# Performance work log

Measured on AMD Instinct MI355X. Metric: run time of the kernel, lower is better.

Reference implementation:

```python
import jax, jax.numpy as jnp
import numpy as np
from math import sqrt

D_MODEL = 1024
N_HEADS = 16
FFN = 4096
B, N = 2, 2048
EPS = 1e-5


def _layernorm(x, g, b):
    mu = jnp.mean(x, -1, keepdims=True)
    var = jnp.mean((x - mu) ** 2, -1, keepdims=True)
    return (x - mu) * jax.lax.rsqrt(var + EPS) * g + b


def setup_inputs() -> dict:
    key = jax.random.key(0)
    ks = jax.random.split(key, 12)
    s = 1.0 / sqrt(D_MODEL)
    sf = 1.0 / sqrt(FFN)
    inp = {
        "tgt": jax.random.normal(ks[0], (B, N, D_MODEL), jnp.float32),
        # True = masked. Causal: query i may attend to keys j <= i.
        "tgt_mask": jnp.triu(jnp.ones((N, N), jnp.bool_), k=1),
        "tgt_key_pad_mask": jnp.zeros((B, N), jnp.bool_),
        "Wq": jax.random.uniform(ks[1], (D_MODEL, D_MODEL), jnp.float32, -s, s),
        "Wk": jax.random.uniform(ks[2], (D_MODEL, D_MODEL), jnp.float32, -s, s),
        "Wv": jax.random.uniform(ks[3], (D_MODEL, D_MODEL), jnp.float32, -s, s),
        "Wo": jax.random.uniform(ks[4], (D_MODEL, D_MODEL), jnp.float32, -s, s),
        "bo": jax.random.uniform(ks[5], (D_MODEL,), jnp.float32, -s, s),
        "W1": jax.random.uniform(ks[6], (FFN, D_MODEL), jnp.float32, -s, s),
        "b1": jax.random.uniform(ks[7], (FFN,), jnp.float32, -s, s),
        "W2": jax.random.uniform(ks[8], (D_MODEL, FFN), jnp.float32, -sf, sf),
        "b2": jax.random.uniform(ks[9], (D_MODEL,), jnp.float32, -sf, sf),
        "g1": jnp.ones((D_MODEL,), jnp.float32),
        "beta1": jnp.zeros((D_MODEL,), jnp.float32),
        "g2": jnp.ones((D_MODEL,), jnp.float32),
        "beta2": jnp.zeros((D_MODEL,), jnp.float32),
    }
    return inp


def _mha(x, tgt_mask, pad_mask, Wq, Wk, Wv, Wo, bo):
    b, n, d = x.shape
    dk = d // N_HEADS
    q = (x @ Wq.T).reshape(b, n, N_HEADS, dk).transpose(0, 2, 1, 3)  # bhnd
    k = (x @ Wk.T).reshape(b, n, N_HEADS, dk).transpose(0, 2, 1, 3)
    v = (x @ Wv.T).reshape(b, n, N_HEADS, dk).transpose(0, 2, 1, 3)
    scores = jnp.einsum("bhqd,bhkd->bhqk", q, k) / sqrt(dk)
    mask = tgt_mask[None, None, :, :] | pad_mask[:, None, None, :]
    scores = jnp.where(mask, -jnp.inf, scores)
    att = jax.nn.softmax(scores, axis=-1)
    out = jnp.einsum("bhqk,bhkd->bhqd", att, v).transpose(0, 2, 1, 3).reshape(b, n, d)
    return out @ Wo.T + bo


def reference(tgt, tgt_mask, tgt_key_pad_mask, Wq, Wk, Wv, Wo, bo,
              W1, b1, W2, b2, g1, beta1, g2, beta2):
    # PostNorm logic (pre_norm=False), dropout=0 (eval)
    h = _mha(tgt, tgt_mask, tgt_key_pad_mask, Wq, Wk, Wv, Wo, bo)
    x = _layernorm(tgt + h, g1, beta1)
    m = jax.nn.gelu(x @ W1.T + b1, approximate=True) @ W2.T + b2
    return _layernorm(x + m, g2, beta2)
```

## Files before the change

kernel.cpp:

```cpp
#include <hip/hip_runtime.h>


#define DEV __device__ __forceinline__

typedef __attribute__((ext_vector_type(4)))  float f32x4;
typedef __attribute__((ext_vector_type(16))) float f32x16;
typedef __attribute__((ext_vector_type(8)))  short s16x8;

static constexpr int Bb   = 2;
static constexpr int NN   = 2048;
static constexpr int DM   = 1024;
static constexpr int HH   = 16;
static constexpr int DK   = 64;
static constexpr int FF   = 4096;
static constexpr int ROWS = Bb * NN;

#define AS1(p) ((const __attribute__((address_space(1))) void*)(p))
#define AS3(p) ((__attribute__((address_space(3))) void*)(p))

DEV unsigned short f2bf(float f) {
  unsigned u = __float_as_uint(f);
  u += 0x7fff + ((u >> 16) & 1);
  return (unsigned short)(u >> 16);
}
DEV float fexp2(float x) {
  float r;
  asm("v_exp_f32 %0, %1" : "=v"(r) : "v"(x));
  return r;
}
DEV unsigned cvtpk(float lo, float hi) {
  unsigned r;
  asm("v_cvt_pk_bf16_f32 %0, %1, %2" : "=v"(r) : "v"(lo), "v"(hi));
  return r;
}

__global__ __launch_bounds__(256) void k_cast7(
    const float* __restrict__ tgt, const float* __restrict__ Wq,
    const float* __restrict__ Wk, const float* __restrict__ Wv,
    const float* __restrict__ Wo, const float* __restrict__ W1,
    const float* __restrict__ W2,
    ushort* __restrict__ xb, ushort* __restrict__ wqb,
    ushort* __restrict__ w1b, ushort* __restrict__ w2b) {
  const int i = blockIdx.x * 256 + threadIdx.x;
  constexpr int S0 = 1048576;
  constexpr int S1 = 262144;
  const float4* src;
  ushort* dstp;
  if (i < S0)               { src = (const float4*)tgt + i;            dstp = xb  + (size_t)i * 4; }
  else if (i < S0 + S1)     { src = (const float4*)Wq + (i - S0);      dstp = wqb + (size_t)(i - S0) * 4; }
  else if (i < S0 + 2 * S1) { src = (const float4*)Wk + (i - S0 - S1); dstp = wqb + (size_t)(i - S0) * 4; }
  else if (i < S0 + 3 * S1) { src = (const float4*)Wv + (i - S0 - 2 * S1); dstp = wqb + (size_t)(i - S0) * 4; }
  else if (i < S0 + 4 * S1) { src = (const float4*)Wo + (i - S0 - 3 * S1); dstp = wqb + (size_t)(i - S0) * 4; }
  else if (i < 3 * S0)      { src = (const float4*)W1 + (i - 2 * S0);  dstp = w1b + (size_t)(i - 2 * S0) * 4; }
  else                      { src = (const float4*)W2 + (i - 3 * S0);  dstp = w2b + (size_t)(i - 3 * S0) * 4; }
  float4 v = *src;
  ushort4 o;
  o.x = f2bf(v.x); o.y = f2bf(v.y); o.z = f2bf(v.z); o.w = f2bf(v.w);
  *reinterpret_cast<ushort4*>(dstp) = o;
}

template <int EPI, int BN, bool QKV>
__global__ __launch_bounds__(256) void k_gemm(
    const ushort* __restrict__ A, const ushort* __restrict__ Bt,
    const float* __restrict__ bias, const float* __restrict__ resid,
    ushort* __restrict__ Cb, float* __restrict__ Cf,
    int K, int nbx) {
  __shared__ ushort As[2][128][32];
  __shared__ ushort Bs[2][BN][32];

  const int t = threadIdx.x;
  const int lane = t & 63, w = t >> 6;
  const int lr = lane & 15, lg = lane >> 4;
  const int lrow = lane >> 2, lc8 = (lane & 3) * 8;

  const int nwg = gridDim.x;
  const int bid = blockIdx.x;
  const int q8 = nwg >> 3, r8 = nwg & 7;
  const int xcd = bid & 7, lin = bid >> 3;
  const int wg = (xcd < r8 ? xcd * (q8 + 1) : r8 * (q8 + 1) + (xcd - r8) * q8) + lin;
  const int band = wg / (4 * nbx);
  const int inn  = wg % (4 * nbx);
  const int by = band * 4 + (inn & 3);
  const int bx = inn >> 2;

  const int bRow = by * 128;
  const int bCol = bx * BN;

  constexpr int NW = BN / 32;
  const int wRow = (w >> 1) * 64, wCol = (w & 1) * (BN / 2);

  const f32x4 zero = {0.f, 0.f, 0.f, 0.f};
  f32x4 acc[4][NW];
#pragma unroll
  for (int m = 0; m < 4; ++m)
#pragma unroll
    for (int n = 0; n < NW; ++n) acc[m][n] = zero;

  auto stage = [&](int buf, int kt) {
#pragma unroll
    for (int i = 0; i < 2; ++i) {
      int rr = w * 32 + i * 16;
      __builtin_amdgcn_global_load_lds(
          AS1(A + (size_t)(bRow + rr + lrow) * K + kt + lc8),
          AS3(&As[buf][rr][0]), 16, 0, 0);
    }
#pragma unroll
    for (int i = 0; i < BN / 64; ++i) {
      int rr = w * (BN / 4) + i * 16;
      __builtin_amdgcn_global_load_lds(
          AS1(Bt + (size_t)(bCol + rr + lrow) * K + kt + lc8),
          AS3(&Bs[buf][rr][0]), 16, 0, 0);
    }
  };

  stage(0, 0);
  const int nk = K / 32;
  for (int tt = 0; tt < nk; ++tt) {
    const int cur = tt & 1;
    __syncthreads();
    if (tt + 1 < nk) stage(cur ^ 1, (tt + 1) * 32);

    s16x8 af[4], bfr[NW];
#pragma unroll
    for (int m = 0; m < 4; ++m)
      af[m] = *reinterpret_cast<const s16x8*>(&As[cur][wRow + m * 16 + lr][lg * 8]);
#pragma unroll
    for (int n = 0; n < NW; ++n)
      bfr[n] = *reinterpret_cast<const s16x8*>(&Bs[cur][wCol + n * 16 + lr][lg * 8]);
#pragma unroll
    for (int m = 0; m < 4; ++m)
#pragma unroll
      for (int n = 0; n < NW; ++n)
        acc[m][n] = __builtin_amdgcn_mfma_f32_16x16x32_bf16(af[m], bfr[n], acc[m][n], 0, 0, 0);
  }

  ushort* CbOut = Cb;
  int colBase = bCol, Ncols = nbx * BN, third = 0;
  if (QKV) {
    third = bCol >> 10;
    CbOut = Cb + (size_t)third * ROWS * DM;
    colBase = bCol & 1023;
    Ncols = DM;
  }
#pragma unroll
  for (int m = 0; m < 4; ++m) {
    int gr = bRow + wRow + m * 16 + lg * 4;
#pragma unroll
    for (int n = 0; n < NW; ++n) {
      int gc = colBase + wCol + n * 16 + lr;
      float bv = (EPI == 1 || EPI == 2) ? bias[gc] : 0.0f;
#pragma unroll
      for (int r = 0; r < 4; ++r) {
        int nr = gr + r;
        float v = acc[m][n][r] + bv;
        if (EPI == 2) {
          size_t idx = (size_t)nr * Ncols + gc;
          Cf[idx] = v + resid[idx];
        } else if (EPI == 1) {
          size_t idx = (size_t)nr * Ncols + gc;
          float u = v + 0.044715f * v * v * v;
          float g = v / (1.0f + __expf(-1.5957691216057308f * u));
          CbOut[idx] = f2bf(g);
        } else {
          int gcs = gc;
          if (QKV && third == 1)
            gcs = (gc & ~63) | ((gc ^ ((nr & 7) << 3)) & 63);
          CbOut[(size_t)nr * Ncols + gcs] = f2bf(v);
        }
      }
    }
  }
}

__global__ __launch_bounds__(256) void k_vt(const ushort* __restrict__ V,
                                            ushort* __restrict__ vT) {
  __shared__ ushort Ls[64][72];
  const int t = threadIdx.x;
  const int n0 = blockIdx.x * 64;
  const int bh = blockIdx.y;
  const int b = bh >> 4, h = bh & 15;
  const int n = t >> 2;
#pragma unroll
  for (int half = 0; half < 2; ++half) {
    int c8 = ((t & 3) + half * 4) * 8;
    int4 v = *reinterpret_cast<const int4*>(
        V + ((size_t)(b * NN + n0 + n)) * DM + h * DK + c8);
    *reinterpret_cast<int4*>(&Ls[n][c8]) = v;
  }
  __syncthreads();
  const int d = t >> 2;
#pragma unroll
  for (int half = 0; half < 2; ++half) {
    int c = (t & 3) + half * 4;
    ushort tmp[8];
#pragma unroll
    for (int j = 0; j < 8; ++j) tmp[j] = Ls[c * 8 + j][d];
    size_t out = ((size_t)bh * DK + d) * NN + n0 + ((c ^ (d & 7)) * 8);
    *reinterpret_cast<int4*>(vT + out) = *reinterpret_cast<const int4*>(tmp);
  }
}

template <int WB>
__global__ __launch_bounds__(256) void k_ln(const float* __restrict__ in,
                                            const float* __restrict__ g,
                                            const float* __restrict__ bta,
                                            float* __restrict__ outf,
                                            ushort* __restrict__ outb) {
  const int row = blockIdx.x;
  const int t = threadIdx.x;
  float4 v = reinterpret_cast<const float4*>(in + (size_t)row * DM)[t];
  float s1 = v.x + v.y + v.z + v.w;
  float s2 = v.x * v.x + v.y * v.y + v.z * v.z + v.w * v.w;
#pragma unroll
  for (int m = 32; m; m >>= 1) {
    s1 += __shfl_xor(s1, m, 64);
    s2 += __shfl_xor(s2, m, 64);
  }
  __shared__ float red[2][4];
  if ((t & 63) == 0) { red[0][t >> 6] = s1; red[1][t >> 6] = s2; }
  __syncthreads();
  s1 = red[0][0] + red[0][1] + red[0][2] + red[0][3];
  s2 = red[1][0] + red[1][1] + red[1][2] + red[1][3];
  const float mu = s1 * (1.0f / DM);
  const float var = s2 * (1.0f / DM) - mu * mu;
  const float rstd = rsqrtf(var + 1e-5f);
  float4 gv = reinterpret_cast<const float4*>(g)[t];
  float4 bv = reinterpret_cast<const float4*>(bta)[t];
  float4 o;
  o.x = (v.x - mu) * rstd * gv.x + bv.x;
  o.y = (v.y - mu) * rstd * gv.y + bv.y;
  o.z = (v.z - mu) * rstd * gv.z + bv.z;
  o.w = (v.w - mu) * rstd * gv.w + bv.w;
  reinterpret_cast<float4*>(outf + (size_t)row * DM)[t] = o;
  if (WB) {
    ushort4 ob;
    ob.x = f2bf(o.x); ob.y = f2bf(o.y); ob.z = f2bf(o.z); ob.w = f2bf(o.w);
    reinterpret_cast<ushort4*>(outb + (size_t)row * DM)[t] = ob;
  }
}

__global__ __launch_bounds__(256) void k_attn(const ushort* __restrict__ Q,
                                              const ushort* __restrict__ Kb,
                                              const ushort* __restrict__ vT,
                                              ushort* __restrict__ O) {
  __shared__ ushort Ks[2][64 * 64];
  __shared__ ushort Vs[2][64 * 64];

  const int t = threadIdx.x;
  const int bid = blockIdx.x;
  const int xcd = bid & 7, j = bid >> 3;
  const int bh = xcd * 4 + (j >> 4);
  const int qi = 15 - (j & 15);
  const int lane = t & 63, wid = t >> 6;
  const int l31 = lane & 31, hi = lane >> 5;
  const int q0w = qi * 128 + wid * 32;
  const size_t qbase = ((size_t)(bh >> 4) * NN) * DM + (bh & 15) * DK;
  const size_t vbase = (size_t)bh * DK * NN;

  const float C = 0.18033688011112043f;

  s16x8 qf[4];
#pragma unroll
  for (int c = 0; c < 4; ++c)
    qf[c] = *reinterpret_cast<const s16x8*>(Q + qbase + (size_t)(q0w + l31) * DM + c * 16 + hi * 8);

  float mrun = -1e30f, lrun = 0.f, negcm = 1e30f;
  f32x16 accO[2];
#pragma unroll
  for (int dt = 0; dt < 2; ++dt)
#pragma unroll
    for (int r = 0; r < 16; ++r) accO[dt][r] = 0.f;

  auto stage = [&](int buf, int kt) {
    const int kk = kt * 64;
#pragma unroll
    for (int i = 0; i < 2; ++i) {
      int row0 = wid * 16 + i * 8;
      __builtin_amdgcn_global_load_lds(
          AS1(Kb + qbase + (size_t)(kk + row0 + (lane >> 3)) * DM + (lane & 7) * 8),
          AS3(&Ks[buf][row0 * 64]), 16, 0, 0);
      __builtin_amdgcn_global_load_lds(
          AS1(vT + vbase + (size_t)(row0 + (lane >> 3)) * NN + kk + (lane & 7) * 8),
          AS3(&Vs[buf][row0 * 64]), 16, 0, 0);
    }
  };

  const int nkt = 2 * qi + 2;
  stage(0, 0);
  for (int kt = 0; kt < nkt; ++kt) {
    const int cur = kt & 1;
    const int kk = kt * 64;
    __syncthreads();
    if (kt + 1 < nkt) stage(cur ^ 1, kt + 1);

    if (kk <= q0w + 31) {
      const char* KsB = (const char*)Ks[cur];
      const char* VsB = (const char*)Vs[cur];
      const bool diag = (kk + 64 > q0w);
      const int nsub = (kk + 32 <= q0w + 31) ? 2 : 1;

      f32x16 st[2];
      __builtin_amdgcn_s_setprio(1);
#pragma unroll
      for (int sub = 0; sub < 2; ++sub) {
        if (sub >= nsub) break;
#pragma unroll
        for (int r = 0; r < 16; ++r) st[sub][r] = 0.f;
        const int row = sub * 32 + l31;
        const int swz = (row & 7) << 4;
#pragma unroll
        for (int c = 0; c < 4; ++c) {
          s16x8 kf = *reinterpret_cast<const s16x8*>(KsB + row * 128 + ((c * 32 + hi * 16) ^ swz));
          st[sub] = __builtin_amdgcn_mfma_f32_32x32x16_bf16(kf, qf[c], st[sub], 0, 0, 0);
        }
      }
      __builtin_amdgcn_s_setprio(0);

      const int q = q0w + l31;
      float p[32];
#pragma unroll
      for (int sub = 0; sub < 2; ++sub) {
        if (sub >= nsub) break;
#pragma unroll
        for (int r = 0; r < 16; ++r) {
          float v = st[sub][r];
          if (diag) {
            int kl = sub * 32 + (r & 3) + 8 * (r >> 2) + 4 * hi;
            if (kk + kl > q) v = -1e30f;
          }
          p[sub * 16 + r] = v;
        }
      }
      float a[16];
#pragma unroll
      for (int i = 0; i < 16; ++i) a[i] = (nsub == 2) ? fmaxf(p[i], p[i + 16]) : p[i];
#pragma unroll
      for (int s = 8; s; s >>= 1)
#pragma unroll
        for (int i = 0; i < 8; ++i) if (i < s) a[i] = fmaxf(a[i], a[i + s]);
      float rm = fmaxf(a[0], __shfl_xor(a[0], 32, 64));

      if (__any(rm > mrun)) {
        const float mn = fmaxf(mrun, rm);
        const float alpha = fexp2(C * (mrun - mn));
        mrun = mn;
        negcm = -C * mn;
        lrun *= alpha;
#pragma unroll
        for (int dt = 0; dt < 2; ++dt) accO[dt] *= alpha;
      }

#pragma unroll
      for (int sub = 0; sub < 2; ++sub) {
        if (sub >= nsub) break;
#pragma unroll
        for (int i = 0; i < 16; ++i)
          p[sub * 16 + i] = fexp2(fmaf(p[sub * 16 + i], C, negcm));
      }
#pragma unroll
      for (int i = 0; i < 16; ++i) a[i] = (nsub == 2) ? (p[i] + p[i + 16]) : p[i];
#pragma unroll
      for (int s = 8; s; s >>= 1)
#pragma unroll
        for (int i = 0; i < 8; ++i) if (i < s) a[i] += a[i + s];
      lrun += a[0] + __shfl_xor(a[0], 32, 64);

      s16x8 pf[4];
#pragma unroll
      for (int sub = 0; sub < 2; ++sub) {
        if (sub >= nsub) break;
#pragma unroll
        for (int hf = 0; hf < 2; ++hf) {
          const float* pp = &p[sub * 16 + hf * 8];
          unsigned X0 = cvtpk(pp[0], pp[1]);
          unsigned X1 = cvtpk(pp[2], pp[3]);
          unsigned Y0 = cvtpk(pp[4], pp[5]);
          unsigned Y1 = cvtpk(pp[6], pp[7]);
          asm volatile("v_permlane32_swap_b32 %0, %1" : "+v"(X0), "+v"(Y0));
          asm volatile("v_permlane32_swap_b32 %0, %1" : "+v"(X1), "+v"(Y1));
          union { unsigned u[4]; s16x8 v; } uu;
          uu.u[0] = X0; uu.u[1] = X1; uu.u[2] = Y0; uu.u[3] = Y1;
          pf[sub * 2 + hf] = uu.v;
        }
      }

      __builtin_amdgcn_s_setprio(1);
#pragma unroll
      for (int dt = 0; dt < 2; ++dt) {
        const int d = dt * 32 + l31;
        const int vswz = (d & 7) << 4;
#pragma unroll
        for (int kc = 0; kc < 4; ++kc) {
          if (kc >= nsub * 2) break;
          s16x8 vf = *reinterpret_cast<const s16x8*>(VsB + d * 128 + ((kc * 32 + hi * 16) ^ vswz));
          accO[dt] = __builtin_amdgcn_mfma_f32_32x32x16_bf16(vf, pf[kc], accO[dt], 0, 0, 0);
        }
      }
      __builtin_amdgcn_s_setprio(0);
    }
  }

  const int q = q0w + l31;
  const float inv = 1.0f / lrun;
#pragma unroll
  for (int dt = 0; dt < 2; ++dt)
#pragma unroll
    for (int rg = 0; rg < 4; ++rg) {
      int d0 = 8 * rg + 4 * hi + 32 * dt;
      ushort4 ov;
      ov.x = f2bf(accO[dt][rg * 4 + 0] * inv);
      ov.y = f2bf(accO[dt][rg * 4 + 1] * inv);
      ov.z = f2bf(accO[dt][rg * 4 + 2] * inv);
      ov.w = f2bf(accO[dt][rg * 4 + 3] * inv);
      *reinterpret_cast<ushort4*>(O + qbase + (size_t)q * DM + d0) = ov;
    }
}

extern "C" void kernel_launch(void* const* d_in, const int* in_sizes, int n_in,
                              void* d_out, int out_size, void* d_ws, size_t ws_size,
                              hipStream_t stream) {
  const float* tgt = (const float*)d_in[0];
  const float* Wq  = (const float*)d_in[3];
  const float* Wk  = (const float*)d_in[4];
  const float* Wv  = (const float*)d_in[5];
  const float* Wo  = (const float*)d_in[6];
  const float* bo  = (const float*)d_in[7];
  const float* W1  = (const float*)d_in[8];
  const float* b1  = (const float*)d_in[9];
  const float* W2  = (const float*)d_in[10];
  const float* b2  = (const float*)d_in[11];
  const float* g1  = (const float*)d_in[12];
  const float* be1 = (const float*)d_in[13];
  const float* g2  = (const float*)d_in[14];
  const float* be2 = (const float*)d_in[15];

  char* ws = (char*)d_ws;
  size_t off = 0;
  auto alloc = [&](size_t bytes) {
    void* p = ws + off;
    off += (bytes + 255) & ~(size_t)255;
    return p;
  };
  ushort* xb   = (ushort*)alloc((size_t)ROWS * DM * 2);
  ushort* wqb  = (ushort*)alloc((size_t)DM * DM * 2);
  ushort* wkb  = (ushort*)alloc((size_t)DM * DM * 2);
  ushort* wvb  = (ushort*)alloc((size_t)DM * DM * 2);
  ushort* wob  = (ushort*)alloc((size_t)DM * DM * 2);
  ushort* w1b  = (ushort*)alloc((size_t)FF * DM * 2);
  ushort* w2b  = (ushort*)alloc((size_t)DM * FF * 2);
  ushort* qbuf = (ushort*)alloc((size_t)ROWS * DM * 2);
  ushort* kbuf = (ushort*)alloc((size_t)ROWS * DM * 2);
  ushort* vbuf = (ushort*)alloc((size_t)ROWS * DM * 2);
  ushort* vtb  = (ushort*)alloc((size_t)ROWS * DM * 2);
  ushort* atnb = (ushort*)alloc((size_t)ROWS * DM * 2);
  float*  h1   = (float*)alloc((size_t)ROWS * DM * 4);
  float*  x1f  = (float*)alloc((size_t)ROWS * DM * 4);
  ushort* x1b  = (ushort*)alloc((size_t)ROWS * DM * 2);
  ushort* t1b  = (ushort*)alloc((size_t)ROWS * FF * 2);
  (void)ws_size; (void)in_sizes; (void)n_in; (void)out_size;
  (void)wkb; (void)wvb; (void)kbuf;

  dim3 blk(256);
  k_cast7<<<dim3(16384), blk, 0, stream>>>(tgt, Wq, Wk, Wv, Wo, W1, W2,
                                           xb, wqb, w1b, w2b);

  k_gemm<0, 128, true><<<dim3(24 * 32), blk, 0, stream>>>(
      xb, wqb, nullptr, nullptr, qbuf, nullptr, DM, 24);

  k_vt<<<dim3(NN / 64, Bb * HH), blk, 0, stream>>>(vbuf, vtb);

  k_attn<<<dim3(512), blk, 0, stream>>>(qbuf, kbuf, vtb, atnb);

  k_gemm<2, 64, false><<<dim3(16 * 32), blk, 0, stream>>>(
      atnb, wob, bo, tgt, nullptr, h1, DM, 16);
  k_ln<1><<<dim3(ROWS), blk, 0, stream>>>(h1, g1, be1, x1f, x1b);

  k_gemm<1, 128, false><<<dim3(32 * 32), blk, 0, stream>>>(
      x1b, w1b, b1, nullptr, t1b, nullptr, DM, 32);
  float* z = h1;
  k_gemm<2, 64, false><<<dim3(16 * 32), blk, 0, stream>>>(
      t1b, w2b, b2, x1f, nullptr, z, FF, 16);
  k_ln<0><<<dim3(ROWS), blk, 0, stream>>>(z, g2, be2, (float*)d_out, nullptr);
}
```

Measured before the change: 290.0 us.

## Split long causal attention tiles across two KV halves and merge partials

The causal attention kernel now uses a 24-entry schedule per head. The eight longest query tiles (qi 8..15) are each split into two blocks that cover halves of the key range. These blocks write unnormalized fp32 partial outputs plus running max and sum to a workspace, and a new merge kernel combines them with log-sum-exp rescaling. This balances per-block work and raises the grid from 512 to 768 blocks, at the cost of an extra launch and extra fp32 partial traffic.

```diff
diff --git a/kernel.cpp b/kernel.cpp
--- a/kernel.cpp
+++ b/kernel.cpp
@@ -239,18 +239,31 @@
   }
 }
 
+static __device__ const unsigned char SCHED24[24][2] = {
+  {15,0},{15,1},{7,2},
+  {14,0},{14,1},{13,0},{13,1},{6,2},
+  {12,0},{12,1},{11,0},{11,1},{5,2},
+  {10,0},{10,1},{9,0},{9,1},{4,2},
+  {8,0},{8,1},{3,2},{2,2},{1,2},{0,2}};
+
 __global__ __launch_bounds__(256) void k_attn(const ushort* __restrict__ Q,
                                               const ushort* __restrict__ Kb,
                                               const ushort* __restrict__ vT,
-                                              ushort* __restrict__ O) {
+                                              ushort* __restrict__ O,
+                                              float* __restrict__ Op,
+                                              float* __restrict__ ml) {
   __shared__ ushort Ks[2][64 * 64];
   __shared__ ushort Vs[2][64 * 64];
 
   const int t = threadIdx.x;
   const int bid = blockIdx.x;
   const int xcd = bid & 7, j = bid >> 3;
-  const int bh = xcd * 4 + (j >> 4);
-  const int qi = 15 - (j & 15);
+  const int head = j / 24, e = j % 24;
+  const int qi = SCHED24[e][0], sv = SCHED24[e][1];
+  const int bh = xcd * 4 + head;
+  const int kt0 = (sv == 1) ? (qi + 1) : 0;
+  const int kt1 = (sv == 0) ? (qi + 1) : (2 * qi + 2);
+
   const int lane = t & 63, wid = t >> 6;
   const int l31 = lane & 31, hi = lane >> 5;
   const int q0w = qi * 128 + wid * 32;
@@ -285,13 +298,12 @@
     }
   };
 
-  const int nkt = 2 * qi + 2;
-  stage(0, 0);
-  for (int kt = 0; kt < nkt; ++kt) {
-    const int cur = kt & 1;
+  stage(0, kt0);
+  for (int kt = kt0, li = 0; kt < kt1; ++kt, ++li) {
+    const int cur = li & 1;
     const int kk = kt * 64;
     __syncthreads();
-    if (kt + 1 < nkt) stage(cur ^ 1, kt + 1);
+    if (kt + 1 < kt1) stage(cur ^ 1, kt + 1);
 
     if (kk <= q0w + 31) {
       const char* KsB = (const char*)Ks[cur];
@@ -400,20 +412,75 @@
     }
   }
 
-  const int q = q0w + l31;
-  const float inv = 1.0f / lrun;
-#pragma unroll
-  for (int dt = 0; dt < 2; ++dt)
-#pragma unroll
-    for (int rg = 0; rg < 4; ++rg) {
-      int d0 = 8 * rg + 4 * hi + 32 * dt;
-      ushort4 ov;
-      ov.x = f2bf(accO[dt][rg * 4 + 0] * inv);
-      ov.y = f2bf(accO[dt][rg * 4 + 1] * inv);
-      ov.z = f2bf(accO[dt][rg * 4 + 2] * inv);
-      ov.w = f2bf(accO[dt][rg * 4 + 3] * inv);
-      *reinterpret_cast<ushort4*>(O + qbase + (size_t)q * DM + d0) = ov;
+  if (sv == 2) {
+    const int q = q0w + l31;
+    const float inv = 1.0f / lrun;
+#pragma unroll
+    for (int dt = 0; dt < 2; ++dt)
+#pragma unroll
+      for (int rg = 0; rg < 4; ++rg) {
+        int d0 = 8 * rg + 4 * hi + 32 * dt;
+        ushort4 ov;
+        ov.x = f2bf(accO[dt][rg * 4 + 0] * inv);
+        ov.y = f2bf(accO[dt][rg * 4 + 1] * inv);
+        ov.z = f2bf(accO[dt][rg * 4 + 2] * inv);
+        ov.w = f2bf(accO[dt][rg * 4 + 3] * inv);
+        *reinterpret_cast<ushort4*>(O + qbase + (size_t)q * DM + d0) = ov;
+      }
+  } else {
+    const int pidx = (bh * 8 + (qi - 8)) * 2 + sv;
+    float* op = Op + (size_t)pidx * (128 * 64);
+    const int row = wid * 32 + l31;
+#pragma unroll
+    for (int dt = 0; dt < 2; ++dt)
+#pragma unroll
+      for (int rg = 0; rg < 4; ++rg) {
+        int d0 = 8 * rg + 4 * hi + 32 * dt;
+        f32x4 v4 = { accO[dt][rg * 4 + 0], accO[dt][rg * 4 + 1],
+                     accO[dt][rg * 4 + 2], accO[dt][rg * 4 + 3] };
+        *reinterpret_cast<f32x4*>(op + (size_t)row * 64 + d0) = v4;
+      }
+    if (hi == 0) {
+      ml[(size_t)pidx * 256 + row * 2 + 0] = mrun;
+      ml[(size_t)pidx * 256 + row * 2 + 1] = lrun;
     }
+  }
+}
+
+__global__ __launch_bounds__(256) void k_amerge(const float* __restrict__ Op,
+                                                const float* __restrict__ ml,
+                                                ushort* __restrict__ O) {
+  const int bh = blockIdx.x >> 3, qq = blockIdx.x & 7;
+  const int t = threadIdx.x;
+  const int row = t >> 1, dh = (t & 1) * 32;
+  const float C = 0.18033688011112043f;
+
+  const int p0 = (bh * 8 + qq) * 2;
+  const float m0 = ml[(size_t)p0 * 256 + row * 2 + 0];
+  const float l0 = ml[(size_t)p0 * 256 + row * 2 + 1];
+  const float m1 = ml[(size_t)(p0 + 1) * 256 + row * 2 + 0];
+  const float l1 = ml[(size_t)(p0 + 1) * 256 + row * 2 + 1];
+  const float M = fmaxf(m0, m1);
+  const float s0 = fexp2(C * (m0 - M));
+  const float s1 = fexp2(C * (m1 - M));
+  const float inv = 1.0f / (l0 * s0 + l1 * s1);
+
+  const float* o0 = Op + (size_t)p0 * (128 * 64) + (size_t)row * 64 + dh;
+  const float* o1 = o0 + 128 * 64;
+  const int b = bh >> 4, h = bh & 15;
+  const int n = (qq + 8) * 128 + row;
+  ushort* dst = O + ((size_t)(b * NN + n)) * DM + h * DK + dh;
+#pragma unroll
+  for (int i = 0; i < 8; ++i) {
+    float4 a = reinterpret_cast<const float4*>(o0)[i];
+    float4 c = reinterpret_cast<const float4*>(o1)[i];
+    ushort4 ov;
+    ov.x = f2bf((a.x * s0 + c.x * s1) * inv);
+    ov.y = f2bf((a.y * s0 + c.y * s1) * inv);
+    ov.z = f2bf((a.z * s0 + c.z * s1) * inv);
+    ov.w = f2bf((a.w * s0 + c.w * s1) * inv);
+    reinterpret_cast<ushort4*>(dst)[i] = ov;
+  }
 }
 
 extern "C" void kernel_launch(void* const* d_in, const int* in_sizes, int n_in,
@@ -457,6 +524,8 @@
   float*  x1f  = (float*)alloc((size_t)ROWS * DM * 4);
   ushort* x1b  = (ushort*)alloc((size_t)ROWS * DM * 2);
   ushort* t1b  = (ushort*)alloc((size_t)ROWS * FF * 2);
+  float*  Opb  = (float*)alloc((size_t)512 * 128 * 64 * 4);
+  float*  mlb  = (float*)alloc((size_t)512 * 256 * 4);
   (void)ws_size; (void)in_sizes; (void)n_in; (void)out_size;
   (void)wkb; (void)wvb; (void)kbuf;
 
@@ -469,7 +538,8 @@
 
   k_vt<<<dim3(NN / 64, Bb * HH), blk, 0, stream>>>(vbuf, vtb);
 
-  k_attn<<<dim3(512), blk, 0, stream>>>(qbuf, kbuf, vtb, atnb);
+  k_attn<<<dim3(768), blk, 0, stream>>>(qbuf, kbuf, vtb, atnb, Opb, mlb);
+  k_amerge<<<dim3(256), blk, 0, stream>>>(Opb, mlb, atnb);
 
   k_gemm<2, 64, false><<<dim3(16 * 32), blk, 0, stream>>>(
       atnb, wob, bo, tgt, nullptr, h1, DM, 16);
```

Measured after the change: 281.6 us. -2.9%, faster.
